# Kernel tuning notes

Measured on AMD Instinct MI355X. Metric: run time of the kernel, lower is better.

Reference implementation:

```python
import jax, jax.numpy as jnp
import numpy as np

N = 100000   # nodes
E = 3200000  # edges
IN = 5
H = 128
L = 6
EPS = 1e-5

def _bn(x, g, b):
    # BatchNorm1d in training mode: batch stats over node dim, biased variance
    m = jnp.mean(x, axis=0)
    v = jnp.mean((x - m) ** 2, axis=0)
    return (x - m) * jax.lax.rsqrt(v + EPS) * g + b

def setup_inputs() -> dict:
    key = jax.random.key(0)
    ks = jax.random.split(key, 20)
    x = jax.random.normal(ks[0], (N, IN), dtype=jnp.float32)
    edge_index = jax.random.randint(ks[1], (2, E), 0, N, dtype=jnp.int64)
    batch = jnp.zeros((N,), dtype=jnp.int64)
    s = 0.05
    return {
        "x": x, "edge_index": edge_index, "batch": batch,
        "in_W": jax.random.normal(ks[2], (IN, H), jnp.float32) * s,
        "in_b": jnp.zeros((H,), jnp.float32),
        "in_g": jnp.ones((H,), jnp.float32),
        "in_beta": jnp.zeros((H,), jnp.float32),
        "conv_W": jax.random.normal(ks[3], (L, H, H), jnp.float32) * s,
        "conv_b": jnp.zeros((L, H), jnp.float32),
        "bn_g": jnp.ones((L, H), jnp.float32),
        "bn_beta": jnp.zeros((L, H), jnp.float32),
        "pW1": jax.random.normal(ks[4], (H, 32), jnp.float32) * s,
        "pb1": jnp.zeros((32,), jnp.float32),
        "pW2": jax.random.normal(ks[5], (32, 1), jnp.float32) * s,
        "pb2": jnp.zeros((1,), jnp.float32),
        "vW1": jax.random.normal(ks[6], (H, 64), jnp.float32) * s,
        "vb1": jnp.zeros((64,), jnp.float32),
        "vW2": jax.random.normal(ks[7], (64, 1), jnp.float32) * s,
        "vb2": jnp.zeros((1,), jnp.float32),
    }

def reference(x, edge_index, batch, in_W, in_b, in_g, in_beta,
              conv_W, conv_b, bn_g, bn_beta,
              pW1, pb1, pW2, pb2, vW1, vb1, vW2, vb2):
    n = x.shape[0]
    # GCN normalization with self-loops (computed once; depends only on edge_index)
    loops = jnp.arange(n, dtype=edge_index.dtype)
    src = jnp.concatenate([edge_index[0], loops])
    dst = jnp.concatenate([edge_index[1], loops])
    deg = jax.ops.segment_sum(jnp.ones_like(dst, dtype=x.dtype), dst, num_segments=n)
    dinv = jnp.where(deg > 0, jax.lax.rsqrt(deg), 0.0)
    norm = dinv[src] * dinv[dst]  # [E+N]

    def gcn(h, W, b):
        h = h @ W
        msg = h[src] * norm[:, None]
        return jax.ops.segment_sum(msg, dst, num_segments=n) + b

    h = jax.nn.relu(_bn(x @ in_W + in_b, in_g, in_beta))
    for i in range(L):
        h = jax.nn.relu(_bn(gcn(h, conv_W[i], conv_b[i]), bn_g[i], bn_beta[i])) + h

    policy_logits = (jax.nn.relu(h @ pW1 + pb1) @ pW2 + pb2)[:, 0]  # [N]

    # global_mean_pool over batch ids (single graph here, num_segments=1)
    num_graphs = 1
    sums = jax.ops.segment_sum(h, batch, num_segments=num_graphs)
    cnts = jax.ops.segment_sum(jnp.ones((n,), h.dtype), batch, num_segments=num_graphs)
    g = sums / jnp.maximum(cnts, 1.0)[:, None]  # [1, H]
    value = jnp.tanh(jax.nn.relu(g @ vW1 + vb1) @ vW2 + vb2)[:, 0]  # [1]
    return policy_logits, value
```

## Files before the change

kernel.cpp:

```cpp
#include <hip/hip_runtime.h>
#include <hip/hip_bf16.h>

typedef __hip_bfloat16 bf16;
typedef long long i64;
typedef unsigned short u16;
typedef __attribute__((ext_vector_type(8))) short bf16x8;
typedef __attribute__((ext_vector_type(4))) float f32x4;
typedef __attribute__((ext_vector_type(2))) long long ll2;

#define EPSV 1e-5f
#define WINLEN 2560
#define CHUNK 64

static __device__ __forceinline__ float ldf(const void* p, size_t i, int fb) {
  return fb ? __bfloat162float(((const bf16*)p)[i]) : ((const float*)p)[i];
}
static __device__ __forceinline__ u16 f2b(float f) {
  unsigned int u = __float_as_uint(f);
  u += 0x7FFF + ((u >> 16) & 1);
  return (u16)(u >> 16);
}
static __device__ __forceinline__ unsigned pk2(float a, float b) {
  return (unsigned)f2b(a) | ((unsigned)f2b(b) << 16);
}
static __device__ __forceinline__ float lo2f(unsigned w) { return __uint_as_float(w << 16); }
static __device__ __forceinline__ float hi2f(unsigned w) { return __uint_as_float(w & 0xFFFF0000u); }


__global__ void setup_kernel(const int* __restrict__ ei_w, const unsigned int* __restrict__ g,
                             int* __restrict__ eflag, int* __restrict__ fflag,
                             int* __restrict__ degcnt,
                             int* __restrict__ wctr, int* __restrict__ pctr,
                             float* __restrict__ buf0, float* __restrict__ buf1,
                             float* __restrict__ ppacc, int n) {
  int i = blockIdx.x * 256 + threadIdx.x;
  if (i < n) degcnt[i] = 0;
  if (blockIdx.x == 0) {
    __shared__ int nz;
    if (threadIdx.x == 0) { nz = 0; *pctr = 0; }
    if (threadIdx.x < 32) wctr[threadIdx.x] = 0;
    buf0[threadIdx.x] = 0.f; buf1[threadIdx.x] = 0.f;
    if (threadIdx.x < 128) ppacc[threadIdx.x] = 0.f;
    __syncthreads();
    for (int k = threadIdx.x; k < 1024; k += 256)
      if (ei_w[2 * k + 1] != 0) atomicAdd(&nz, 1);
    __syncthreads();
    if (threadIdx.x == 0) {
      *eflag = (nz == 0) ? 1 : 0;
      *fflag = (g[0] == 0x3F803F80u) ? 1 : 0;
    }
  }
}


__global__ void __launch_bounds__(256) pre_merged_kernel(
    const void* __restrict__ x, const void* __restrict__ W, const void* __restrict__ b,
    const void* __restrict__ ei, const void* __restrict__ convW,
    const int* __restrict__ eflag, const int* __restrict__ fflag,
    int* __restrict__ degcnt, u16* __restrict__ pre, float* __restrict__ acc0,
    u16* __restrict__ wf, int n, int in_dim, int e, int wtotal, int gi, int gf) {
  __shared__ float4 SS[256], QQ[256];
  int fb = *fflag;
  if ((int)blockIdx.x < gi) {
    int q = threadIdx.x & 31, g8 = threadIdx.x >> 5;
    int c = q * 4;
    float b0 = ldf(b, c, fb), b1 = ldf(b, c + 1, fb), b2v = ldf(b, c + 2, fb), b3 = ldf(b, c + 3, fb);
    float s0 = 0, s1 = 0, s2 = 0, s3 = 0, q0 = 0, q1 = 0, q2 = 0, q3 = 0;
    for (int node = blockIdx.x * 8 + g8; node < n; node += gi * 8) {
      float a0 = b0, a1 = b1, a2 = b2v, a3 = b3;
      for (int k = 0; k < in_dim; ++k) {
        float xv = ldf(x, (size_t)node * in_dim + k, fb);
        size_t w0 = (size_t)k * 128 + c;
        a0 = fmaf(xv, ldf(W, w0, fb), a0);
        a1 = fmaf(xv, ldf(W, w0 + 1, fb), a1);
        a2 = fmaf(xv, ldf(W, w0 + 2, fb), a2);
        a3 = fmaf(xv, ldf(W, w0 + 3, fb), a3);
      }
      unsigned w0p = pk2(a0, a1), w1p = pk2(a2, a3);
      *(uint2*)(pre + (size_t)node * 128 + c) = make_uint2(w0p, w1p);
      float r0 = lo2f(w0p), r1 = hi2f(w0p), r2 = lo2f(w1p), r3 = hi2f(w1p);
      s0 += r0; s1 += r1; s2 += r2; s3 += r3;
      q0 = fmaf(r0, r0, q0); q1 = fmaf(r1, r1, q1); q2 = fmaf(r2, r2, q2); q3 = fmaf(r3, r3, q3);
    }
    SS[threadIdx.x] = make_float4(s0, s1, s2, s3);
    QQ[threadIdx.x] = make_float4(q0, q1, q2, q3);
    __syncthreads();
    if (threadIdx.x < 32) {
      float4 a = SS[threadIdx.x], qq = QQ[threadIdx.x];
      for (int g2 = 1; g2 < 8; ++g2) {
        float4 u = SS[g2 * 32 + threadIdx.x], w = QQ[g2 * 32 + threadIdx.x];
        a.x += u.x; a.y += u.y; a.z += u.z; a.w += u.w;
        qq.x += w.x; qq.y += w.y; qq.z += w.z; qq.w += w.w;
      }
      int cc = threadIdx.x * 4;
      atomicAdd(&acc0[cc + 0], a.x); atomicAdd(&acc0[cc + 1], a.y);
      atomicAdd(&acc0[cc + 2], a.z); atomicAdd(&acc0[cc + 3], a.w);
      atomicAdd(&acc0[128 + cc + 0], qq.x); atomicAdd(&acc0[128 + cc + 1], qq.y);
      atomicAdd(&acc0[128 + cc + 2], qq.z); atomicAdd(&acc0[128 + cc + 3], qq.w);
    }
  } else if ((int)blockIdx.x < gi + gf) {
    int bid = blockIdx.x - gi;
    int k = bid & 7;
    int lo = (int)(((long long)n * k) >> 3);
    int hi = (int)(((long long)n * (k + 1)) >> 3);
    int stride = (gf >> 3) * 256;
    int fb64 = *eflag;
    for (int i = (bid >> 3) * 256 + threadIdx.x; i < e; i += stride) {
      int d;
      if (fb64) d = (int)((const i64*)ei)[(size_t)e + i];
      else      d = ((const int*)ei)[(size_t)e + i];
      if (d >= lo && d < hi) atomicAdd(&degcnt[d], 1);
    }
  } else {
    int bid = blockIdx.x - gi - gf;
    int i = bid * 256 + threadIdx.x;
    if (i < wtotal) {
      int l = i >> 14, r = i & 16383;
      int k = r >> 7, nn = r & 127;
      int s = k >> 5, quad = (k >> 3) & 3, j = k & 7;
      int ct = nn >> 4, n16 = nn & 15;
      wf[(size_t)l * 16384 + (ct * 4 + s) * 512 + quad * 128 + n16 * 8 + j] = f2b(ldf(convW, i, fb));
    }
  }
}


__global__ void __launch_bounds__(256) scanA_kernel(const int* __restrict__ deg,
                                                    int* __restrict__ rp,
                                                    int* __restrict__ bsum,
                                                    float* __restrict__ dinv, int n) {
  int base = blockIdx.x * 1024 + threadIdx.x * 4;
  int v0 = (base     < n) ? deg[base]     : 0;
  int v1 = (base + 1 < n) ? deg[base + 1] : 0;
  int v2 = (base + 2 < n) ? deg[base + 2] : 0;
  int v3 = (base + 3 < n) ? deg[base + 3] : 0;
  if (base     < n) dinv[base]     = rsqrtf((float)v0 + 1.0f);
  if (base + 1 < n) dinv[base + 1] = rsqrtf((float)v1 + 1.0f);
  if (base + 2 < n) dinv[base + 2] = rsqrtf((float)v2 + 1.0f);
  if (base + 3 < n) dinv[base + 3] = rsqrtf((float)v3 + 1.0f);
  int ts = v0 + v1 + v2 + v3;
  __shared__ int ls[256];
  ls[threadIdx.x] = ts;
  __syncthreads();
  for (int off = 1; off < 256; off <<= 1) {
    int u = (threadIdx.x >= off) ? ls[threadIdx.x - off] : 0;
    __syncthreads();
    ls[threadIdx.x] += u;
    __syncthreads();
  }
  int run = ls[threadIdx.x] - ts;
  if (base     < n) rp[base]     = run; run += v0;
  if (base + 1 < n) rp[base + 1] = run; run += v1;
  if (base + 2 < n) rp[base + 2] = run; run += v2;
  if (base + 3 < n) rp[base + 3] = run;
  if (threadIdx.x == 255) bsum[blockIdx.x] = ls[255];
}

__global__ void __launch_bounds__(256) scanB_kernel(int* __restrict__ bsum, int* __restrict__ rp,
                                                    int nb, int n, int e) {
  __shared__ int ls[256];
  int t = threadIdx.x;
  int v = (t < nb) ? bsum[t] : 0;
  ls[t] = v;
  __syncthreads();
  for (int off = 1; off < 256; off <<= 1) {
    int u = (t >= off) ? ls[t - off] : 0;
    __syncthreads();
    ls[t] += u;
    __syncthreads();
  }
  if (t < nb) bsum[t] = ls[t] - v;
  if (t == 0) rp[n] = e;
}

__global__ void scanC_kernel(int* __restrict__ rp, const int* __restrict__ bsum,
                             int* __restrict__ rpw, int n) {
  int i = blockIdx.x * 256 + threadIdx.x;
  if (i < n) {
    int v = rp[i] + bsum[i >> 10];
    rp[i] = v;
    rpw[i] = v;
  }
}

__global__ void fill_kernel(const void* __restrict__ ei, const int* __restrict__ flag,
                            int* __restrict__ rpw, int* __restrict__ csr_src, int e, int n) {
  int k = blockIdx.x & 7;
  int lo = (int)(((long long)n * k) >> 3);
  int hi = (int)(((long long)n * (k + 1)) >> 3);
  int stride = (gridDim.x >> 3) * 1024;
  int fb64 = *flag;
  for (int i = (blockIdx.x >> 3) * 1024 + threadIdx.x * 4; i < e; i += stride) {
    if (i + 3 < e) {
      int d0, d1, d2, d3;
      if (fb64) {
        ll2 a = *(const ll2*)((const i64*)ei + (size_t)e + i);
        ll2 b2 = *(const ll2*)((const i64*)ei + (size_t)e + i + 2);
        d0 = (int)a.x; d1 = (int)a.y; d2 = (int)b2.x; d3 = (int)b2.y;
      } else {
        int4 dv = *(const int4*)((const int*)ei + (size_t)e + i);
        d0 = dv.x; d1 = dv.y; d2 = dv.z; d3 = dv.w;
      }
      int in0 = (d0 >= lo && d0 < hi), in1 = (d1 >= lo && d1 < hi);
      int in2 = (d2 >= lo && d2 < hi), in3 = (d3 >= lo && d3 < hi);
      if (in0 | in1 | in2 | in3) {
        int s0, s1, s2, s3;
        if (fb64) {
          ll2 sa = *(const ll2*)((const i64*)ei + i);
          ll2 sb = *(const ll2*)((const i64*)ei + i + 2);
          s0 = (int)sa.x; s1 = (int)sa.y; s2 = (int)sb.x; s3 = (int)sb.y;
        } else {
          int4 sv = *(const int4*)((const int*)ei + i);
          s0 = sv.x; s1 = sv.y; s2 = sv.z; s3 = sv.w;
        }
        if (in0) { int pos = atomicAdd(&rpw[d0], 1); csr_src[pos] = s0; }
        if (in1) { int pos = atomicAdd(&rpw[d1], 1); csr_src[pos] = s1; }
        if (in2) { int pos = atomicAdd(&rpw[d2], 1); csr_src[pos] = s2; }
        if (in3) { int pos = atomicAdd(&rpw[d3], 1); csr_src[pos] = s3; }
      }
    } else {
      for (int j = 0; i + j < e; ++j) {
        int d = fb64 ? (int)((const i64*)ei)[(size_t)e + i + j] : ((const int*)ei)[(size_t)e + i + j];
        if (d < lo || d >= hi) continue;
        int s = fb64 ? (int)((const i64*)ei)[i + j] : ((const int*)ei)[i + j];
        int pos = atomicAdd(&rpw[d], 1);
        csr_src[pos] = s;
      }
    }
  }
}


__global__ void __launch_bounds__(256) gemm_bn_kernel(
    const u16* __restrict__ pre, u16* __restrict__ hbuf,
    const float* __restrict__ accIn, float* __restrict__ accZ,
    const void* __restrict__ g, const void* __restrict__ beta, const int* __restrict__ fflag,
    const u16* __restrict__ wfL, const float* __restrict__ dinv,
    u16* __restrict__ u, int n, int use_res, float inv_n, int gOff) {
  __shared__ u16 At[4][2048];
  __shared__ float SC[128], SH[128];
  int fb = *fflag;
  if (threadIdx.x < 128) {
    int c = threadIdx.x;
    float s = accIn[c], s2 = accIn[128 + c];
    float mean = s * inv_n;
    float var = s2 * inv_n - mean * mean;
    float sc = ldf(g, (size_t)gOff + c, fb) * rsqrtf(var + EPSV);
    SC[c] = sc;
    SH[c] = ldf(beta, (size_t)gOff + c, fb) - mean * sc;
  }
  if (blockIdx.x == 0) accZ[threadIdx.x] = 0.f;
  __syncthreads();

  int lane = threadIdx.x & 63;
  int wave = threadIdx.x >> 6;
  int n16 = lane & 15, quad = lane >> 4;
  u16* at = At[wave];
  int node = lane & 15;
  int cgrp = lane >> 4;
  int ntiles = (n + 15) >> 4;
  for (int tile = blockIdx.x * 4 + wave; tile < ntiles; tile += gridDim.x * 4) {
    int n0 = tile * 16;
    int gn = n0 + node;
#pragma unroll
    for (int r = 0; r < 4; ++r) {
      int c8 = r * 4 + cgrp;
      int c = c8 * 8;
      uint4 ww = make_uint4(0u, 0u, 0u, 0u);
      if (gn < n) {
        uint4 pv = *(const uint4*)(pre + (size_t)gn * 128 + c);
        unsigned pw[4] = {pv.x, pv.y, pv.z, pv.w};
        float h[8];
#pragma unroll
        for (int m = 0; m < 4; ++m) {
          h[2 * m]     = fmaxf(fmaf(lo2f(pw[m]), SC[c + 2 * m],     SH[c + 2 * m]), 0.f);
          h[2 * m + 1] = fmaxf(fmaf(hi2f(pw[m]), SC[c + 2 * m + 1], SH[c + 2 * m + 1]), 0.f);
        }
        if (use_res) {
          uint4 rv = *(const uint4*)(hbuf + (size_t)gn * 128 + c);
          unsigned rw[4] = {rv.x, rv.y, rv.z, rv.w};
#pragma unroll
          for (int m = 0; m < 4; ++m) {
            h[2 * m] += lo2f(rw[m]); h[2 * m + 1] += hi2f(rw[m]);
          }
        }
        ww.x = pk2(h[0], h[1]); ww.y = pk2(h[2], h[3]);
        ww.z = pk2(h[4], h[5]); ww.w = pk2(h[6], h[7]);
        *(uint4*)(hbuf + (size_t)gn * 128 + c) = ww;
      }
      int c4 = c8 * 2;
      int s = c4 >> 3, qd = (c4 >> 1) & 3;
      *(uint4*)(at + s * 512 + qd * 128 + node * 8) = ww;
    }
    __builtin_amdgcn_s_waitcnt(0);
    f32x4 acc[8];
#pragma unroll
    for (int ct = 0; ct < 8; ++ct) acc[ct] = (f32x4){0.f, 0.f, 0.f, 0.f};
#pragma unroll
    for (int s = 0; s < 4; ++s) {
      bf16x8 af = *(const bf16x8*)(at + s * 512 + lane * 8);
#pragma unroll
      for (int ct = 0; ct < 8; ++ct) {
        bf16x8 bfr = *(const bf16x8*)(wfL + (size_t)(ct * 4 + s) * 512 + lane * 8);
        acc[ct] = __builtin_amdgcn_mfma_f32_16x16x32_bf16(af, bfr, acc[ct], 0, 0, 0);
      }
    }
    float dv[4];
#pragma unroll
    for (int r = 0; r < 4; ++r) {
      int row = n0 + quad * 4 + r;
      dv[r] = (row < n) ? dinv[row] : 0.f;
    }
#pragma unroll
    for (int ct = 0; ct < 8; ++ct) {
#pragma unroll
      for (int r = 0; r < 4; ++r) {
        int row = n0 + quad * 4 + r;
        if (row < n)
          u[((size_t)(ct >> 1) * n + row) * 32 + (ct & 1) * 16 + n16] = f2b(acc[ct][r] * dv[r]);
      }
    }
  }
}


__global__ void __launch_bounds__(256) gather_stats_kernel(
    const int* __restrict__ row_ptr, const int* __restrict__ csr_src,
    const u16* __restrict__ u, const float* __restrict__ dinv,
    const void* __restrict__ b, const int* __restrict__ fflag,
    u16* __restrict__ pre, float* __restrict__ accOut,
    int* __restrict__ wctr, int n, int nch, size_t bOff) {
  __shared__ int sm[WINLEN];
  __shared__ float SW[4][4][8], QW[4][4][8];
  __shared__ int curchunk;
  int fb = *fflag;
  int ct2 = blockIdx.x & 3;
  const u16* us = u + (size_t)ct2 * n * 32;
  int q = threadIdx.x & 3;
  int g = threadIdx.x >> 2;
  int c = ct2 * 32 + q * 8;
  float bias[8];
#pragma unroll
  for (int i = 0; i < 8; ++i) bias[i] = ldf(b, bOff + c + i, fb);
  float sA[8], qA[8];
#pragma unroll
  for (int i = 0; i < 8; ++i) { sA[i] = 0.f; qA[i] = 0.f; }

  for (;;) {
    __syncthreads();
    if (threadIdx.x == 0) curchunk = atomicAdd(&wctr[ct2], 1);
    __syncthreads();
    int ch = curchunk;
    if (ch >= nch) break;
    int c0 = ch * CHUNK;
    int node = c0 + g;
    int valid = node < n;
    int beg = valid ? row_ptr[node] : 0;
    int end = valid ? row_ptr[node + 1] : 0;
    int cend = c0 + CHUNK; if (cend > n) cend = n;
    int chunk_lo = row_ptr[c0];
    int chunk_hi = row_ptr[cend];
    float acc[8];
    if (valid) {
      uint4 su = *(const uint4*)(us + (size_t)node * 32 + q * 8);
      acc[0] = lo2f(su.x); acc[1] = hi2f(su.x);
      acc[2] = lo2f(su.y); acc[3] = hi2f(su.y);
      acc[4] = lo2f(su.z); acc[5] = hi2f(su.z);
      acc[6] = lo2f(su.w); acc[7] = hi2f(su.w);
    } else {
#pragma unroll
      for (int i = 0; i < 8; ++i) acc[i] = 0.f;
    }
    for (int wlo = chunk_lo; wlo < chunk_hi; wlo += WINLEN) {
      int wlen = chunk_hi - wlo; if (wlen > WINLEN) wlen = WINLEN;
      __syncthreads();
      for (int i = threadIdx.x; i < wlen; i += 256)
        sm[i] = __builtin_nontemporal_load(csr_src + wlo + i);
      __syncthreads();
      int j0 = beg > wlo ? beg : wlo;
      int j1 = end < wlo + wlen ? end : wlo + wlen;
      int j = j0;
#define ACC(UU) \
      acc[0] += lo2f(UU.x); acc[1] += hi2f(UU.x); \
      acc[2] += lo2f(UU.y); acc[3] += hi2f(UU.y); \
      acc[4] += lo2f(UU.z); acc[5] += hi2f(UU.z); \
      acc[6] += lo2f(UU.w); acc[7] += hi2f(UU.w);
      for (; j + 8 <= j1; j += 8) {
        int i0 = sm[j - wlo],     i1 = sm[j - wlo + 1], i2 = sm[j - wlo + 2], i3 = sm[j - wlo + 3];
        int i4 = sm[j - wlo + 4], i5 = sm[j - wlo + 5], i6 = sm[j - wlo + 6], i7 = sm[j - wlo + 7];
        uint4 U0 = *(const uint4*)(us + (size_t)i0 * 32 + q * 8);
        uint4 U1 = *(const uint4*)(us + (size_t)i1 * 32 + q * 8);
        uint4 U2 = *(const uint4*)(us + (size_t)i2 * 32 + q * 8);
        uint4 U3 = *(const uint4*)(us + (size_t)i3 * 32 + q * 8);
        uint4 U4 = *(const uint4*)(us + (size_t)i4 * 32 + q * 8);
        uint4 U5 = *(const uint4*)(us + (size_t)i5 * 32 + q * 8);
        uint4 U6 = *(const uint4*)(us + (size_t)i6 * 32 + q * 8);
        uint4 U7 = *(const uint4*)(us + (size_t)i7 * 32 + q * 8);
        ACC(U0) ACC(U1) ACC(U2) ACC(U3) ACC(U4) ACC(U5) ACC(U6) ACC(U7)
      }
      for (; j + 4 <= j1; j += 4) {
        int i0 = sm[j - wlo], i1 = sm[j - wlo + 1], i2 = sm[j - wlo + 2], i3 = sm[j - wlo + 3];
        uint4 U0 = *(const uint4*)(us + (size_t)i0 * 32 + q * 8);
        uint4 U1 = *(const uint4*)(us + (size_t)i1 * 32 + q * 8);
        uint4 U2 = *(const uint4*)(us + (size_t)i2 * 32 + q * 8);
        uint4 U3 = *(const uint4*)(us + (size_t)i3 * 32 + q * 8);
        ACC(U0) ACC(U1) ACC(U2) ACC(U3)
      }
      for (; j < j1; ++j) {
        int i0 = sm[j - wlo];
        uint4 U0 = *(const uint4*)(us + (size_t)i0 * 32 + q * 8);
        ACC(U0)
      }
#undef ACC
    }
    if (valid) {
      float dv = dinv[node];
      float o0 = fmaf(acc[0], dv, bias[0]), o1 = fmaf(acc[1], dv, bias[1]);
      float o2 = fmaf(acc[2], dv, bias[2]), o3 = fmaf(acc[3], dv, bias[3]);
      float o4 = fmaf(acc[4], dv, bias[4]), o5 = fmaf(acc[5], dv, bias[5]);
      float o6 = fmaf(acc[6], dv, bias[6]), o7 = fmaf(acc[7], dv, bias[7]);
      unsigned w0 = pk2(o0, o1), w1 = pk2(o2, o3), w2 = pk2(o4, o5), w3 = pk2(o6, o7);
      *(uint4*)(pre + (size_t)node * 128 + c) = make_uint4(w0, w1, w2, w3);
      float r0 = lo2f(w0), r1 = hi2f(w0), r2 = lo2f(w1), r3 = hi2f(w1);
      float r4 = lo2f(w2), r5 = hi2f(w2), r6 = lo2f(w3), r7 = hi2f(w3);
      sA[0] += r0; sA[1] += r1; sA[2] += r2; sA[3] += r3;
      sA[4] += r4; sA[5] += r5; sA[6] += r6; sA[7] += r7;
      qA[0] = fmaf(r0, r0, qA[0]); qA[1] = fmaf(r1, r1, qA[1]);
      qA[2] = fmaf(r2, r2, qA[2]); qA[3] = fmaf(r3, r3, qA[3]);
      qA[4] = fmaf(r4, r4, qA[4]); qA[5] = fmaf(r5, r5, qA[5]);
      qA[6] = fmaf(r6, r6, qA[6]); qA[7] = fmaf(r7, r7, qA[7]);
    }
  }
#pragma unroll
  for (int m = 4; m <= 32; m <<= 1) {
#pragma unroll
    for (int i = 0; i < 8; ++i) {
      sA[i] += __shfl_xor(sA[i], m, 64);
      qA[i] += __shfl_xor(qA[i], m, 64);
    }
  }
  int lane = threadIdx.x & 63, wv = threadIdx.x >> 6;
  if (lane < 4) {
#pragma unroll
    for (int i = 0; i < 8; ++i) { SW[wv][lane][i] = sA[i]; QW[wv][lane][i] = qA[i]; }
  }
  __syncthreads();
  if (threadIdx.x < 32) {
    int qq = threadIdx.x >> 3, i = threadIdx.x & 7;
    float a = SW[0][qq][i] + SW[1][qq][i] + SW[2][qq][i] + SW[3][qq][i];
    float b2 = QW[0][qq][i] + QW[1][qq][i] + QW[2][qq][i] + QW[3][qq][i];
    int chn = ct2 * 32 + qq * 8 + i;
    atomicAdd(&accOut[chn], a);
    atomicAdd(&accOut[128 + chn], b2);
  }
}


__global__ void __launch_bounds__(256) policy_pool_kernel(
    const u16* __restrict__ pre, const u16* __restrict__ hbuf,
    const float* __restrict__ accIn,
    const void* __restrict__ bg, const void* __restrict__ bbeta, int gOff,
    const void* __restrict__ pW1, const void* __restrict__ pb1,
    const void* __restrict__ pW2, const void* __restrict__ pb2,
    const void* __restrict__ vW1, const void* __restrict__ vb1,
    const void* __restrict__ vW2, const void* __restrict__ vb2,
    const int* __restrict__ fflag, float* __restrict__ ppacc, int* __restrict__ pctr,
    void* __restrict__ out, int n, float inv_n) {
  __shared__ float W1[128 * 32];
  __shared__ float B1v[32], W2v[32];
  __shared__ float SC[128], SH[128];
  __shared__ int plast;
  int fb = *fflag;
  for (int i = threadIdx.x; i < 128 * 32; i += 256) W1[i] = ldf(pW1, i, fb);
  if (threadIdx.x < 32) {
    B1v[threadIdx.x] = ldf(pb1, threadIdx.x, fb);
    W2v[threadIdx.x] = ldf(pW2, threadIdx.x, fb);
  }
  if (threadIdx.x < 128) {
    int cch = threadIdx.x;
    float s = accIn[cch], s2 = accIn[128 + cch];
    float mean = s * inv_n;
    float var = s2 * inv_n - mean * mean;
    float sc = ldf(bg, (size_t)gOff + cch, fb) * rsqrtf(var + EPSV);
    SC[cch] = sc;
    SH[cch] = ldf(bbeta, (size_t)gOff + cch, fb) - mean * sc;
  }
  __syncthreads();
  float bias2 = ldf(pb2, 0, fb);
  int q = threadIdx.x & 31, g8 = threadIdx.x >> 5;
  int c = q * 4;
  float4 sc = *(const float4*)&SC[c];
  float4 sh = *(const float4*)&SH[c];
  float cs0 = 0, cs1 = 0, cs2 = 0, cs3 = 0;
  for (int node = blockIdx.x * 8 + g8; node < n; node += gridDim.x * 8) {
    uint2 pv = *(const uint2*)(pre + (size_t)node * 128 + c);
    uint2 rv = *(const uint2*)(hbuf + (size_t)node * 128 + c);
    float4 h4;
    h4.x = fmaxf(fmaf(lo2f(pv.x), sc.x, sh.x), 0.f) + lo2f(rv.x);
    h4.y = fmaxf(fmaf(hi2f(pv.x), sc.y, sh.y), 0.f) + hi2f(rv.x);
    h4.z = fmaxf(fmaf(lo2f(pv.y), sc.z, sh.z), 0.f) + lo2f(rv.y);
    h4.w = fmaxf(fmaf(hi2f(pv.y), sc.w, sh.w), 0.f) + hi2f(rv.y);
    cs0 += h4.x; cs1 += h4.y; cs2 += h4.z; cs3 += h4.w;
    float acc = B1v[q];
#pragma unroll
    for (int k4 = 0; k4 < 32; ++k4) {
      float hx = __shfl(h4.x, k4, 32);
      float hy = __shfl(h4.y, k4, 32);
      float hz = __shfl(h4.z, k4, 32);
      float hw = __shfl(h4.w, k4, 32);
      int k = k4 * 4;
      acc = fmaf(hx, W1[k * 32 + q], acc);
      acc = fmaf(hy, W1[(k + 1) * 32 + q], acc);
      acc = fmaf(hz, W1[(k + 2) * 32 + q], acc);
      acc = fmaf(hw, W1[(k + 3) * 32 + q], acc);
    }
    acc = fmaxf(acc, 0.f) * W2v[q];
    for (int off = 16; off; off >>= 1) acc += __shfl_down(acc, off, 32);
    if (q == 0) {
      float v = acc + bias2;
      if (fb) ((bf16*)out)[node] = __float2bfloat16(v);
      else    ((float*)out)[node] = v;
    }
  }
  __shared__ float4 SS[256];
  SS[threadIdx.x] = make_float4(cs0, cs1, cs2, cs3);
  __syncthreads();
  if (threadIdx.x < 32) {
    float4 a = SS[threadIdx.x];
    for (int g2 = 1; g2 < 8; ++g2) {
      float4 u = SS[g2 * 32 + threadIdx.x];
      a.x += u.x; a.y += u.y; a.z += u.z; a.w += u.w;
    }
    int cc = threadIdx.x * 4;
    atomicAdd(&ppacc[cc + 0], a.x); atomicAdd(&ppacc[cc + 1], a.y);
    atomicAdd(&ppacc[cc + 2], a.z); atomicAdd(&ppacc[cc + 3], a.w);
  }
  __syncthreads();
  if (threadIdx.x == 0) {
    int old = atomicAdd(pctr, 1);
    plast = (old == (int)gridDim.x - 1) ? 1 : 0;
  }
  __syncthreads();
  if (plast) {
    __shared__ float gs[128];
    if (threadIdx.x < 128) gs[threadIdx.x] = atomicAdd(&ppacc[threadIdx.x], 0.f);
    __syncthreads();
    if (threadIdx.x < 64) {
      int cc = threadIdx.x;
      float acc2 = ldf(vb1, cc, fb);
      for (int k = 0; k < 128; ++k)
        acc2 = fmaf(gs[k] * inv_n, ldf(vW1, (size_t)k * 64 + cc, fb), acc2);
      acc2 = fmaxf(acc2, 0.f);
      float v = acc2 * ldf(vW2, cc, fb);
      for (int off = 32; off; off >>= 1) v += __shfl_down(v, off, 64);
      if (cc == 0) {
        float rr = tanhf(v + ldf(vb2, 0, fb));
        if (fb) ((bf16*)out)[n] = __float2bfloat16(rr);
        else    ((float*)out)[n] = rr;
      }
    }
  }
}


extern "C" void kernel_launch(void* const* d_in, const int* in_sizes, int n_in,
                              void* d_out, int out_size, void* d_ws, size_t ws_size,
                              hipStream_t stream) {
  const void* x       = d_in[0];
  const void* ei      = d_in[1];
  const void* in_W    = d_in[3];
  const void* in_b    = d_in[4];
  const void* in_g    = d_in[5];
  const void* in_beta = d_in[6];
  const void* conv_W  = d_in[7];
  const void* conv_b  = d_in[8];
  const void* bn_g    = d_in[9];
  const void* bn_beta = d_in[10];
  const void* pW1     = d_in[11];
  const void* pb1     = d_in[12];
  const void* pW2     = d_in[13];
  const void* pb2     = d_in[14];
  const void* vW1     = d_in[15];
  const void* vb1     = d_in[16];
  const void* vW2     = d_in[17];
  const void* vb2     = d_in[18];

  const int H = 128;
  int in_dim = in_sizes[3] / H;
  int n      = in_sizes[0] / in_dim;
  int e      = in_sizes[1] / 2;
  int L      = in_sizes[7] / (H * H);

  const int GS  = 2048;
  const int GI  = 512;
  const int GP  = 1024;
  const int GF  = 2048;

  char* w = (char*)d_ws;
  u16*   u    = (u16*)w;   w += (size_t)n * H * sizeof(u16);
  u16*   pre  = (u16*)w;   w += (size_t)n * H * sizeof(u16);
  u16*   hbuf = (u16*)w;   w += (size_t)n * H * sizeof(u16);
  int*   csr_src  = (int*)w;   w += ((size_t)e + 16) * sizeof(int);
  int*   row_ptr  = (int*)w;   w += (size_t)(n + 1 + 15) / 16 * 16 * sizeof(int);
  int*   degcnt   = (int*)w;   w += (size_t)n * sizeof(int);
  int*   rpw      = (int*)w;   w += (size_t)n * sizeof(int);
  float* dinv     = (float*)w; w += (size_t)n * sizeof(float);
  int*   eflag = (int*)w;   w += 16 * sizeof(int);
  int*   fflag = (int*)w;   w += 16 * sizeof(int);
  int*   bsum  = (int*)w;   w += 256 * sizeof(int);
  int*   wctr  = (int*)w;   w += 32 * sizeof(int);
  int*   pctr  = (int*)w;   w += 16 * sizeof(int);
  float* buf0  = (float*)w; w += 256 * sizeof(float);
  float* buf1  = (float*)w; w += 256 * sizeof(float);
  float* ppacc = (float*)w; w += 128 * sizeof(float);
  u16*   wf    = (u16*)w;   w += (size_t)L * H * H * sizeof(u16);

  int gN = (n + 255) / 256;
  int nb = (n + 1023) >> 10;
  int nch = (n + CHUNK - 1) / CHUNK;
  int wtotal = L * H * H;
  int GW = (wtotal + 255) / 256;
  float inv_n = 1.0f / (float)n;
  float* bufs[2] = {buf0, buf1};

  setup_kernel<<<gN, 256, 0, stream>>>((const int*)ei, (const unsigned int*)in_g,
                                       eflag, fflag, degcnt, wctr, pctr,
                                       buf0, buf1, ppacc, n);
  pre_merged_kernel<<<GI + GF + GW, 256, 0, stream>>>(
      x, in_W, in_b, ei, conv_W, eflag, fflag, degcnt, pre, buf0, wf,
      n, in_dim, e, wtotal, GI, GF);
  scanA_kernel<<<nb, 256, 0, stream>>>(degcnt, row_ptr, bsum, dinv, n);
  scanB_kernel<<<1, 256, 0, stream>>>(bsum, row_ptr, nb, n, e);
  scanC_kernel<<<gN, 256, 0, stream>>>(row_ptr, bsum, rpw, n);
  fill_kernel<<<GF, 256, 0, stream>>>(ei, eflag, rpw, csr_src, e, n);

  for (int l = 0; l < L; ++l) {
    const void* g    = (l == 0) ? in_g    : bn_g;
    const void* beta = (l == 0) ? in_beta : bn_beta;
    int gOff = (l == 0) ? 0 : (l - 1) * H;
    gemm_bn_kernel<<<2048, 256, 0, stream>>>(pre, hbuf, bufs[l & 1], bufs[(l + 1) & 1],
                                             g, beta, fflag, wf + (size_t)l * H * H,
                                             dinv, u, n, (l > 0) ? 1 : 0, inv_n, gOff);
    gather_stats_kernel<<<GS, 256, 0, stream>>>(row_ptr, csr_src, u, dinv,
                                                conv_b, fflag, pre, bufs[(l + 1) & 1],
                                                wctr + l * 4, n, nch, (size_t)l * H);
  }

  policy_pool_kernel<<<GP, 256, 0, stream>>>(pre, hbuf, bufs[L & 1],
                                             bn_g, bn_beta, (L - 1) * H,
                                             pW1, pb1, pW2, pb2, vW1, vb1, vW2, vb2,
                                             fflag, ppacc, pctr, d_out, n, inv_n);
}
```

Before: 1.677 ms.

## Replicate BN stat accumulators across slots and stage GEMM output through LDS

Spreads the global atomic accumulators for batch-norm sums, squared sums and the pooled sum over eight replicated slots chosen by block index, and consumers add the slots back together. The aim is to cut same-address atomic contention from thousands of blocks. Separately, the GEMM epilogue now writes its bf16 results into shared memory and then stores 16-byte vectors to global memory, replacing scattered 2-byte stores. The cost is a few extra reads in the prologue and extra LDS traffic, and the staging buffer is reused without a barrier, which relies on per-wave ordering.

```diff
diff --git a/kernel.cpp b/kernel.cpp
--- a/kernel.cpp
+++ b/kernel.cpp
@@ -11,6 +11,7 @@
 #define EPSV 1e-5f
 #define WINLEN 2560
 #define CHUNK 64
+#define NREP 8
 
 static __device__ __forceinline__ float ldf(const void* p, size_t i, int fb) {
   return fb ? __bfloat162float(((const bf16*)p)[i]) : ((const float*)p)[i];
@@ -39,8 +40,8 @@
     __shared__ int nz;
     if (threadIdx.x == 0) { nz = 0; *pctr = 0; }
     if (threadIdx.x < 32) wctr[threadIdx.x] = 0;
-    buf0[threadIdx.x] = 0.f; buf1[threadIdx.x] = 0.f;
-    if (threadIdx.x < 128) ppacc[threadIdx.x] = 0.f;
+    for (int k = threadIdx.x; k < NREP * 256; k += 256) { buf0[k] = 0.f; buf1[k] = 0.f; }
+    for (int k = threadIdx.x; k < NREP * 128; k += 256) ppacc[k] = 0.f;
     __syncthreads();
     for (int k = threadIdx.x; k < 1024; k += 256)
       if (ei_w[2 * k + 1] != 0) atomicAdd(&nz, 1);
@@ -92,11 +93,12 @@
         a.x += u.x; a.y += u.y; a.z += u.z; a.w += u.w;
         qq.x += w.x; qq.y += w.y; qq.z += w.z; qq.w += w.w;
       }
+      float* ar = acc0 + (blockIdx.x & (NREP - 1)) * 256;
       int cc = threadIdx.x * 4;
-      atomicAdd(&acc0[cc + 0], a.x); atomicAdd(&acc0[cc + 1], a.y);
-      atomicAdd(&acc0[cc + 2], a.z); atomicAdd(&acc0[cc + 3], a.w);
-      atomicAdd(&acc0[128 + cc + 0], qq.x); atomicAdd(&acc0[128 + cc + 1], qq.y);
-      atomicAdd(&acc0[128 + cc + 2], qq.z); atomicAdd(&acc0[128 + cc + 3], qq.w);
+      atomicAdd(&ar[cc + 0], a.x); atomicAdd(&ar[cc + 1], a.y);
+      atomicAdd(&ar[cc + 2], a.z); atomicAdd(&ar[cc + 3], a.w);
+      atomicAdd(&ar[128 + cc + 0], qq.x); atomicAdd(&ar[128 + cc + 1], qq.y);
+      atomicAdd(&ar[128 + cc + 2], qq.z); atomicAdd(&ar[128 + cc + 3], qq.w);
     }
   } else if ((int)blockIdx.x < gi + gf) {
     int bid = blockIdx.x - gi;
@@ -242,14 +244,20 @@
   int fb = *fflag;
   if (threadIdx.x < 128) {
     int c = threadIdx.x;
-    float s = accIn[c], s2 = accIn[128 + c];
+    float s = 0.f, s2 = 0.f;
+#pragma unroll
+    for (int r = 0; r < NREP; ++r) {
+      s  += accIn[r * 256 + c];
+      s2 += accIn[r * 256 + 128 + c];
+    }
     float mean = s * inv_n;
     float var = s2 * inv_n - mean * mean;
     float sc = ldf(g, (size_t)gOff + c, fb) * rsqrtf(var + EPSV);
     SC[c] = sc;
     SH[c] = ldf(beta, (size_t)gOff + c, fb) - mean * sc;
   }
-  if (blockIdx.x == 0) accZ[threadIdx.x] = 0.f;
+  if (blockIdx.x == 0)
+    for (int i = threadIdx.x; i < NREP * 256; i += 256) accZ[i] = 0.f;
   __syncthreads();
 
   int lane = threadIdx.x & 63;
@@ -315,9 +323,19 @@
     for (int ct = 0; ct < 8; ++ct) {
 #pragma unroll
       for (int r = 0; r < 4; ++r) {
-        int row = n0 + quad * 4 + r;
-        if (row < n)
-          u[((size_t)(ct >> 1) * n + row) * 32 + (ct & 1) * 16 + n16] = f2b(acc[ct][r] * dv[r]);
+        at[(ct >> 1) * 512 + (quad * 4 + r) * 32 + (ct & 1) * 16 + n16] = f2b(acc[ct][r] * dv[r]);
+      }
+    }
+    __builtin_amdgcn_s_waitcnt(0);
+#pragma unroll
+    for (int it = 0; it < 4; ++it) {
+      int f = it * 512 + lane * 8;
+      int nd = (f >> 5) & 15;
+      int ch = f & 31;
+      int row = n0 + nd;
+      if (row < n) {
+        uint4 vv = *(const uint4*)(at + f);
+        *(uint4*)(u + ((size_t)it * n + row) * 32 + ch) = vv;
       }
     }
   }
@@ -450,8 +468,9 @@
     float a = SW[0][qq][i] + SW[1][qq][i] + SW[2][qq][i] + SW[3][qq][i];
     float b2 = QW[0][qq][i] + QW[1][qq][i] + QW[2][qq][i] + QW[3][qq][i];
     int chn = ct2 * 32 + qq * 8 + i;
-    atomicAdd(&accOut[chn], a);
-    atomicAdd(&accOut[128 + chn], b2);
+    float* ar = accOut + (blockIdx.x & (NREP - 1)) * 256;
+    atomicAdd(&ar[chn], a);
+    atomicAdd(&ar[128 + chn], b2);
   }
 }
 
@@ -478,7 +497,12 @@
   }
   if (threadIdx.x < 128) {
     int cch = threadIdx.x;
-    float s = accIn[cch], s2 = accIn[128 + cch];
+    float s = 0.f, s2 = 0.f;
+#pragma unroll
+    for (int r = 0; r < NREP; ++r) {
+      s  += accIn[r * 256 + cch];
+      s2 += accIn[r * 256 + 128 + cch];
+    }
     float mean = s * inv_n;
     float var = s2 * inv_n - mean * mean;
     float sc = ldf(bg, (size_t)gOff + cch, fb) * rsqrtf(var + EPSV);
@@ -531,9 +555,10 @@
       float4 u = SS[g2 * 32 + threadIdx.x];
       a.x += u.x; a.y += u.y; a.z += u.z; a.w += u.w;
     }
+    float* pr = ppacc + (blockIdx.x & (NREP - 1)) * 128;
     int cc = threadIdx.x * 4;
-    atomicAdd(&ppacc[cc + 0], a.x); atomicAdd(&ppacc[cc + 1], a.y);
-    atomicAdd(&ppacc[cc + 2], a.z); atomicAdd(&ppacc[cc + 3], a.w);
+    atomicAdd(&pr[cc + 0], a.x); atomicAdd(&pr[cc + 1], a.y);
+    atomicAdd(&pr[cc + 2], a.z); atomicAdd(&pr[cc + 3], a.w);
   }
   __syncthreads();
   if (threadIdx.x == 0) {
@@ -543,7 +568,13 @@
   __syncthreads();
   if (plast) {
     __shared__ float gs[128];
-    if (threadIdx.x < 128) gs[threadIdx.x] = atomicAdd(&ppacc[threadIdx.x], 0.f);
+    if (threadIdx.x < 128) {
+      float t = 0.f;
+#pragma unroll
+      for (int r = 0; r < NREP; ++r)
+        t += atomicAdd(&ppacc[r * 128 + threadIdx.x], 0.f);
+      gs[threadIdx.x] = t;
+    }
     __syncthreads();
     if (threadIdx.x < 64) {
       int cc = threadIdx.x;
@@ -610,9 +641,9 @@
   int*   bsum  = (int*)w;   w += 256 * sizeof(int);
   int*   wctr  = (int*)w;   w += 32 * sizeof(int);
   int*   pctr  = (int*)w;   w += 16 * sizeof(int);
-  float* buf0  = (float*)w; w += 256 * sizeof(float);
-  float* buf1  = (float*)w; w += 256 * sizeof(float);
-  float* ppacc = (float*)w; w += 128 * sizeof(float);
+  float* buf0  = (float*)w; w += (size_t)NREP * 256 * sizeof(float);
+  float* buf1  = (float*)w; w += (size_t)NREP * 256 * sizeof(float);
+  float* ppacc = (float*)w; w += (size_t)NREP * 128 * sizeof(float);
   u16*   wf    = (u16*)w;   w += (size_t)L * H * H * sizeof(u16);
 
   int gN = (n + 255) / 256;
```

After: 1.538 ms. 8.3% less time.
